# Kernel tuning notes

Measured on AMD Instinct MI355X. Metric: run time of the kernel, lower is better.

The kernel has to match this reference:

```python
import jax, jax.numpy as jnp
import numpy as np

ITEM_SIZE = 100000
USER_SIZE = 1000000
K = 64
B = 1048576


def setup_inputs() -> dict:
    key = jax.random.key(0)
    k1, k2, k3, k4, k5, k6 = jax.random.split(key, 6)
    u = jax.random.randint(k1, (B,), 0, USER_SIZE, dtype=jnp.int64 if jax.config.read('jax_enable_x64') else jnp.int32)
    i = jax.random.randint(k2, (B,), 0, ITEM_SIZE, dtype=u.dtype)
    s = jax.random.randint(k3, (B,), 0, 2, dtype=u.dtype)
    # xavier_normal-style init (gain=1): std = sqrt(2/(fan_in+fan_out))
    diff = jax.random.normal(k4, (ITEM_SIZE, 1), dtype=jnp.float32) * np.sqrt(2.0 / (ITEM_SIZE + 1))
    disc = jax.random.normal(k5, (ITEM_SIZE, K), dtype=jnp.float32) * np.sqrt(2.0 / (ITEM_SIZE + K))
    theta = jax.random.normal(k6, (USER_SIZE, K), dtype=jnp.float32) * np.sqrt(2.0 / (USER_SIZE + K))
    return {"u": u, "i": i, "s": s, "diff": diff, "disc": disc, "theta": theta}


def reference(u, i, s, diff, disc, theta):
    # Original computes eye(B) * (disc[i] @ theta[u].T) then sums rows:
    # that is exactly the per-pair dot product, computed here directly.
    disc_i = disc[i]            # [B, k] gather
    theta_u = theta[u]          # [B, k] gather
    x = jnp.sum(disc_i * theta_u, axis=1, keepdims=True) + diff[i]  # [B, 1]
    real = s.astype(jnp.float32)[:, None]                            # [B, 1]
    # BCE(sigmoid(x), real), numerically stable via log_sigmoid
    loss = -jnp.mean(real * jax.nn.log_sigmoid(x) + (1.0 - real) * jax.nn.log_sigmoid(-x))
    return loss
```

## Files before the change

kernel.cpp:

```cpp
#include <hip/hip_runtime.h>


#define GRID_BLOCKS 4096

__global__ __launch_bounds__(256) void mirt_partial_kernel(
    const int* __restrict__ u,
    const int* __restrict__ iidx,
    const int* __restrict__ s,
    const float* __restrict__ diff,
    const float* __restrict__ disc,
    const float* __restrict__ theta,
    float* __restrict__ partials,
    int B)
{
    const int lane16 = threadIdx.x & 15;
    const int groupInBlock = threadIdx.x >> 4;
    const int groupsPerBlock = blockDim.x >> 4;
    const int stride = gridDim.x * groupsPerBlock;
    int pair = blockIdx.x * groupsPerBlock + groupInBlock;

    int uu = 0, ii = 0, ss = 0;
    if (pair < B) { uu = u[pair]; ii = iidx[pair]; ss = s[pair]; }

    float acc = 0.0f;
    for (; pair < B; ) {
        const int npair = pair + stride;
        int nuu = 0, nii = 0, nss = 0;
        if (npair < B) {
            nuu = u[npair];
            nii = iidx[npair];
            nss = s[npair];
        }
        const float4 t4 = ((const float4*)(theta + (size_t)uu * 64))[lane16];
        const float4 d4 = ((const float4*)(disc  + (size_t)ii * 64))[lane16];
        const float df  = diff[ii];
        float p = t4.x * d4.x + t4.y * d4.y + t4.z * d4.z + t4.w * d4.w;
        p += __shfl_xor(p, 1);
        p += __shfl_xor(p, 2);
        p += __shfl_xor(p, 4);
        p += __shfl_xor(p, 8);
        if (lane16 == 0) {
            const float x = p + df;
            const float z = (ss != 0) ? -x : x;
            acc += fmaxf(z, 0.0f) + log1pf(__expf(-fabsf(z)));
        }
        pair = npair; uu = nuu; ii = nii; ss = nss;
    }

    acc += __shfl_xor(acc, 32);
    acc += __shfl_xor(acc, 16);
    acc += __shfl_xor(acc, 8);
    acc += __shfl_xor(acc, 4);
    acc += __shfl_xor(acc, 2);
    acc += __shfl_xor(acc, 1);

    __shared__ float wave_sums[4];
    const int wave = threadIdx.x >> 6;
    const int lane = threadIdx.x & 63;
    if (lane == 0) wave_sums[wave] = acc;
    __syncthreads();
    if (threadIdx.x == 0) {
        partials[blockIdx.x] =
            wave_sums[0] + wave_sums[1] + wave_sums[2] + wave_sums[3];
    }
}

__global__ __launch_bounds__(256) void mirt_final_kernel(
    const float* __restrict__ partials, float* __restrict__ out,
    int n, float inv_b)
{
    float acc = 0.0f;
    for (int j = threadIdx.x; j < n; j += 256) acc += partials[j];

    acc += __shfl_xor(acc, 32);
    acc += __shfl_xor(acc, 16);
    acc += __shfl_xor(acc, 8);
    acc += __shfl_xor(acc, 4);
    acc += __shfl_xor(acc, 2);
    acc += __shfl_xor(acc, 1);

    __shared__ float wave_sums[4];
    const int wave = threadIdx.x >> 6;
    const int lane = threadIdx.x & 63;
    if (lane == 0) wave_sums[wave] = acc;
    __syncthreads();
    if (threadIdx.x == 0) {
        out[0] = (wave_sums[0] + wave_sums[1] + wave_sums[2] + wave_sums[3])
                 * inv_b;
    }
}

extern "C" void kernel_launch(void* const* d_in, const int* in_sizes, int n_in,
                              void* d_out, int out_size, void* d_ws, size_t ws_size,
                              hipStream_t stream) {
    const int*   u     = (const int*)d_in[0];
    const int*   iidx  = (const int*)d_in[1];
    const int*   s     = (const int*)d_in[2];
    const float* diff  = (const float*)d_in[3];
    const float* disc  = (const float*)d_in[4];
    const float* theta = (const float*)d_in[5];
    float* out      = (float*)d_out;
    float* partials = (float*)d_ws;

    const int B = in_sizes[0];

    mirt_partial_kernel<<<GRID_BLOCKS, 256, 0, stream>>>(
        u, iidx, s, diff, disc, theta, partials, B);
    mirt_final_kernel<<<1, 256, 0, stream>>>(
        partials, out, GRID_BLOCKS, 1.0f / (float)B);
}
```

Measured before the change: 392.0 us.

## Launch one pair per 16-lane group with 65536 blocks instead of grid-stride loop

Replaces the grid-stride loop, which prefetched the next pair's indices, with a flat launch of 65536 blocks where each 16-lane group handles exactly one pair. The aim is more memory-level parallelism for the random gathers from theta and disc, since many more independent loads can be in flight at once. The per-block reduction is trimmed to two shuffles because only lane 0 of each group holds a value. The final reduction now reads 65536 partials with float4 loads across 1024 threads. The cost is a larger partials buffer and more block scheduling overhead.

```diff
diff --git a/kernel.cpp b/kernel.cpp
--- a/kernel.cpp
+++ b/kernel.cpp
@@ -1,7 +1,7 @@
 #include <hip/hip_runtime.h>
 
 
-#define GRID_BLOCKS 4096
+#define S1_BLOCKS 65536
 
 __global__ __launch_bounds__(256) void mirt_partial_kernel(
     const int* __restrict__ u,
@@ -14,23 +14,14 @@
     int B)
 {
     const int lane16 = threadIdx.x & 15;
-    const int groupInBlock = threadIdx.x >> 4;
-    const int groupsPerBlock = blockDim.x >> 4;
-    const int stride = gridDim.x * groupsPerBlock;
-    int pair = blockIdx.x * groupsPerBlock + groupInBlock;
-
-    int uu = 0, ii = 0, ss = 0;
-    if (pair < B) { uu = u[pair]; ii = iidx[pair]; ss = s[pair]; }
+    const int group  = threadIdx.x >> 4;
+    const int pair   = (blockIdx.x << 4) + group;
 
     float acc = 0.0f;
-    for (; pair < B; ) {
-        const int npair = pair + stride;
-        int nuu = 0, nii = 0, nss = 0;
-        if (npair < B) {
-            nuu = u[npair];
-            nii = iidx[npair];
-            nss = s[npair];
-        }
+    if (pair < B) {
+        const int uu = u[pair];
+        const int ii = iidx[pair];
+        const int ss = s[pair];
         const float4 t4 = ((const float4*)(theta + (size_t)uu * 64))[lane16];
         const float4 d4 = ((const float4*)(disc  + (size_t)ii * 64))[lane16];
         const float df  = diff[ii];
@@ -42,9 +33,31 @@
         if (lane16 == 0) {
             const float x = p + df;
             const float z = (ss != 0) ? -x : x;
-            acc += fmaxf(z, 0.0f) + log1pf(__expf(-fabsf(z)));
+            acc = fmaxf(z, 0.0f) + log1pf(__expf(-fabsf(z)));
         }
-        pair = npair; uu = nuu; ii = nii; ss = nss;
+    }
+
+    acc += __shfl_xor(acc, 16);
+    acc += __shfl_xor(acc, 32);
+
+    __shared__ float wave_sums[4];
+    const int wave = threadIdx.x >> 6;
+    if ((threadIdx.x & 63) == 0) wave_sums[wave] = acc;
+    __syncthreads();
+    if (threadIdx.x == 0)
+        partials[blockIdx.x] =
+            (wave_sums[0] + wave_sums[1]) + (wave_sums[2] + wave_sums[3]);
+}
+
+__global__ __launch_bounds__(1024) void mirt_final_kernel(
+    const float* __restrict__ partials, float* __restrict__ out,
+    int n4, float inv_b)
+{
+    const float4* p4 = (const float4*)partials;
+    float acc = 0.0f;
+    for (int j = threadIdx.x; j < n4; j += 1024) {
+        const float4 v = p4[j];
+        acc += (v.x + v.y) + (v.z + v.w);
     }
 
     acc += __shfl_xor(acc, 32);
@@ -54,39 +67,16 @@
     acc += __shfl_xor(acc, 2);
     acc += __shfl_xor(acc, 1);
 
-    __shared__ float wave_sums[4];
+    __shared__ float wave_sums[16];
     const int wave = threadIdx.x >> 6;
     const int lane = threadIdx.x & 63;
     if (lane == 0) wave_sums[wave] = acc;
     __syncthreads();
     if (threadIdx.x == 0) {
-        partials[blockIdx.x] =
-            wave_sums[0] + wave_sums[1] + wave_sums[2] + wave_sums[3];
-    }
-}
-
-__global__ __launch_bounds__(256) void mirt_final_kernel(
-    const float* __restrict__ partials, float* __restrict__ out,
-    int n, float inv_b)
-{
-    float acc = 0.0f;
-    for (int j = threadIdx.x; j < n; j += 256) acc += partials[j];
-
-    acc += __shfl_xor(acc, 32);
-    acc += __shfl_xor(acc, 16);
-    acc += __shfl_xor(acc, 8);
-    acc += __shfl_xor(acc, 4);
-    acc += __shfl_xor(acc, 2);
-    acc += __shfl_xor(acc, 1);
-
-    __shared__ float wave_sums[4];
-    const int wave = threadIdx.x >> 6;
-    const int lane = threadIdx.x & 63;
-    if (lane == 0) wave_sums[wave] = acc;
-    __syncthreads();
-    if (threadIdx.x == 0) {
-        out[0] = (wave_sums[0] + wave_sums[1] + wave_sums[2] + wave_sums[3])
-                 * inv_b;
+        float t = 0.0f;
+        #pragma unroll
+        for (int w = 0; w < 16; ++w) t += wave_sums[w];
+        out[0] = t * inv_b;
     }
 }
 
@@ -104,8 +94,8 @@
 
     const int B = in_sizes[0];
 
-    mirt_partial_kernel<<<GRID_BLOCKS, 256, 0, stream>>>(
+    mirt_partial_kernel<<<S1_BLOCKS, 256, 0, stream>>>(
         u, iidx, s, diff, disc, theta, partials, B);
-    mirt_final_kernel<<<1, 256, 0, stream>>>(
-        partials, out, GRID_BLOCKS, 1.0f / (float)B);
+    mirt_final_kernel<<<1, 1024, 0, stream>>>(
+        partials, out, S1_BLOCKS / 4, 1.0f / (float)B);
 }
```

Measured after the change: 401.1 us. +2.3%, slower.
